# Kernel tuning notes

Measured on AMD Instinct MI355X. Metric: run time of the kernel, lower is better.

The kernel has to match this reference:

```python
import jax, jax.numpy as jnp
import numpy as np

B, Q, HIST, HID, NH, D, BS, NBLK, NUMB = 8, 512, 1536, 4096, 32, 128, 64, 32, 256


def _rope(x, pos):
    # GPT-NeoX-style rotary used by Falcon: rotate_half over full head_dim.
    Dh = x.shape[-1]
    inv = 1.0 / (10000.0 ** (jnp.arange(0, Dh, 2, dtype=jnp.float32) / Dh))  # [D/2]
    ang = pos.astype(jnp.float32)[:, None] * inv[None, :]                    # [T, D/2]
    cos = jnp.concatenate([jnp.cos(ang), jnp.cos(ang)], -1)[None, :, None, :]
    sin = jnp.concatenate([jnp.sin(ang), jnp.sin(ang)], -1)[None, :, None, :]
    half = Dh // 2
    rot = jnp.concatenate([-x[..., half:], x[..., :half]], -1)
    return x * cos + rot * sin


def setup_inputs() -> dict:
    key = jax.random.key(0)
    ks = jax.random.split(key, 6)
    hidden_states = jax.random.normal(ks[0], (1, B * Q, HID), jnp.float32) * 0.02
    qkv_weight = jax.random.normal(ks[1], ((NH + 2) * D, HID), jnp.float32) * 0.02
    dense_weight = jax.random.normal(ks[2], (HID, NH * D), jnp.float32) * 0.02
    past_key = jax.random.normal(ks[3], (NUMB, BS, 1, D), jnp.float32) * 0.02
    past_value = jax.random.normal(ks[4], (NUMB, BS, 1, D), jnp.float32) * 0.02
    q_start_loc = (jnp.arange(B) * Q).astype(jnp.int32)
    q_seq_length = jnp.full((B,), Q, jnp.int32)
    history_lengths = jnp.full((B,), HIST, jnp.int32)
    # each sequence owns NBLK distinct cache blocks (shuffled block table)
    block_offsets = jax.random.permutation(ks[5], NUMB).reshape(B, NBLK).astype(jnp.int32)
    position_ids_1d = (history_lengths[:, None] + jnp.arange(Q, dtype=jnp.int32)[None, :]).reshape(-1)
    return dict(hidden_states=hidden_states, qkv_weight=qkv_weight, dense_weight=dense_weight,
                past_key=past_key, past_value=past_value, q_start_loc=q_start_loc,
                q_seq_length=q_seq_length, history_lengths=history_lengths,
                block_offsets=block_offsets, position_ids_1d=position_ids_1d)


def reference(hidden_states, qkv_weight, dense_weight, past_key, past_value,
              q_start_loc, q_seq_length, history_lengths, block_offsets, position_ids_1d):
    T = hidden_states.shape[1]
    Bn = block_offsets.shape[0]
    Qn = T // Bn
    Dh = past_key.shape[-1]
    BSz = past_key.shape[1]
    # fused QKV projection
    fused = hidden_states @ qkv_weight.T                      # [1, T, (NH+2)*D]
    NHh = fused.shape[-1] // Dh - 2
    qkv = fused.reshape(1, T, NHh + 2, Dh)
    q = qkv[:, :, :NHh]                                       # [1, T, NH, D]
    k = qkv[:, :, NHh:NHh + 1]                                 # [1, T, 1, D]
    v = qkv[:, :, NHh + 1:]                                    # [1, T, 1, D]
    # inline rotary embedding on q, k
    q = _rope(q, position_ids_1d)
    k = _rope(k, position_ids_1d)
    # fill_kv_cache: scatter new K/V into paged cache via block table
    seq_id = jnp.repeat(jnp.arange(Bn), Qn)                   # [T]
    pos = position_ids_1d.astype(jnp.int32)                   # absolute kv position
    blk = block_offsets[seq_id, pos // BSz]                   # [T] physical block id
    off = pos % BSz
    past_key = past_key.at[blk, off].set(k.reshape(T, 1, Dh))
    past_value = past_value.at[blk, off].set(v.reshape(T, 1, Dh))
    # paged_attention_fwd: gather per-sequence K/V from paged cache
    KVc = block_offsets.shape[1] * BSz                        # kv capacity == kv_len here
    kseq = past_key[block_offsets].reshape(Bn, KVc, Dh)       # [B, KV, D] (1 kv head squeezed)
    vseq = past_value[block_offsets].reshape(Bn, KVc, Dh)
    qb = q.reshape(Bn, Qn, NHh, Dh)
    scale = 1.0 / jnp.sqrt(jnp.float32(Dh))
    scores = jnp.einsum('bqhd,bkd->bhqk', qb, kseq) * scale   # [B, H, Q, KV]
    qpos = history_lengths[:, None] + jnp.arange(Qn)[None, :] # [B, Q]
    mask = jnp.arange(KVc)[None, None, :] <= qpos[:, :, None] # causal + length mask
    scores = jnp.where(mask[:, None, :, :], scores, jnp.float32(-1e30))
    attn = jax.nn.softmax(scores, axis=-1)
    out = jnp.einsum('bhqk,bkd->bqhd', attn, vseq)            # [B, Q, H, D]
    out = out.reshape(1, T, NHh * Dh)
    return out @ dense_weight.T                                # [1, T, hidden]
```

## Files before the change

kernel.cpp:

```cpp
#include <hip/hip_runtime.h>

typedef __attribute__((ext_vector_type(8))) short bf16x8;
typedef __attribute__((ext_vector_type(4))) float f32x4;
typedef __attribute__((ext_vector_type(16))) float f32x16;
typedef __attribute__((ext_vector_type(2))) unsigned int u32x2;

constexpr int B_ = 8, Q_ = 512, HIST_ = 1536, HID_ = 4096, NH_ = 32, D_ = 128;
constexpr int BS_ = 64, NBLK_ = 32;
constexpr int T_ = B_ * Q_;
constexpr int QKVN = (NH_ + 2) * D_;
constexpr int KVC = NBLK_ * BS_;

__device__ __forceinline__ unsigned short f2bf(float f) {
  union { float f; unsigned u; } v; v.f = f;
  unsigned r = v.u + 0x7FFFu + ((v.u >> 16) & 1u);
  return (unsigned short)(r >> 16);
}
__device__ __forceinline__ float bf2f(unsigned short s) {
  union { unsigned u; float f; } v; v.u = ((unsigned)s) << 16;
  return v.f;
}
__device__ __forceinline__ int cvtpk_bf16(float lo, float hi) {
  int r;
  asm("v_cvt_pk_bf16_f32 %0, %1, %2" : "=v"(r) : "v"(lo), "v"(hi));
  return r;
}

__global__ void k_conv(const float* __restrict__ in, unsigned short* __restrict__ out, int n4) {
  int i = blockIdx.x * blockDim.x + threadIdx.x;
  int stride = gridDim.x * blockDim.x;
  for (; i < n4; i += stride) {
    float4 v = reinterpret_cast<const float4*>(in)[i];
    ushort4 o;
    o.x = f2bf(v.x); o.y = f2bf(v.y); o.z = f2bf(v.z); o.w = f2bf(v.w);
    reinterpret_cast<ushort4*>(out)[i] = o;
  }
}

__global__ __launch_bounds__(512, 2) void k_gemm256(const unsigned short* __restrict__ A,
                          const unsigned short* __restrict__ Bm,
                          float* __restrict__ Cf, unsigned short* __restrict__ Cb,
                          int MB, int K, int ldc) {
  extern __shared__ unsigned short smem[];
  unsigned short* sA = smem;
  unsigned short* sB = smem + 32768;
  const int tid = threadIdx.x, lane = tid & 63, w = tid >> 6;
  const int wr = w >> 2, wc = w & 3;
  const int lr = lane & 15, lk = lane >> 4;

  const int nwg = gridDim.x, orig = blockIdx.x;
  const int q8 = nwg >> 3, r8 = nwg & 7, xcd = orig & 7;
  const int wg = (xcd < r8 ? xcd * (q8 + 1) : r8 * (q8 + 1) + (xcd - r8) * q8) + (orig >> 3);
  const int m0 = (wg % MB) * 256;
  const int n0 = (wg / MB) * 256;
  const int NT = K >> 6;

  f32x4 acc[8][4];
#pragma unroll
  for (int mf = 0; mf < 8; ++mf)
#pragma unroll
    for (int nf = 0; nf < 4; ++nf) acc[mf][nf] = f32x4{0.f, 0.f, 0.f, 0.f};

  auto stage = [&](const unsigned short* __restrict__ Mat, int rbase, unsigned short* regionBase,
                   int ts, int half) {
    const int di = ts < NT ? ts : NT - 1;
    const size_t k0 = (size_t)di << 6;
    char* hb = (char*)(regionBase + (ts & 1) * 16384 + half * 8192);
#pragma unroll
    for (int c = 0; c < 2; ++c) {
      const int ob = c * 8192 + (w << 10) + (lane << 4);
      const int row = ob >> 7;
      const int sl = ((ob >> 4) & 7) ^ (row & 7);
      const unsigned short* src = Mat + (size_t)(rbase + half * 128 + row) * K + k0 + sl * 8;
      __builtin_amdgcn_global_load_lds((const __attribute__((address_space(1))) void*)src,
          (__attribute__((address_space(3))) void*)(hb + c * 8192 + (w << 10)), 16, 0, 0);
    }
  };

  stage(A, m0, sA, 0, 0); stage(A, m0, sA, 0, 1);
  stage(Bm, n0, sB, 0, 0); stage(Bm, n0, sB, 0, 1);
  stage(Bm, n0, sB, 1, 0); stage(Bm, n0, sB, 1, 1);
  asm volatile("s_waitcnt vmcnt(4)" ::: "memory");
  __builtin_amdgcn_s_barrier();

  for (int t = 0; t < NT; ++t) {
    const int cur = t & 1;
    unsigned short* a_t = sA + cur * 16384 + wr * 8192;
    unsigned short* b_t = sB + cur * 16384 + (wc >> 1) * 8192;
    bf16x8 bfr[4][2];
#pragma unroll
    for (int p = 0; p < 4; ++p) {
      bf16x8 af[2][2];
#pragma unroll
      for (int m = 0; m < 2; ++m)
#pragma unroll
        for (int kk = 0; kk < 2; ++kk) {
          const int r = p * 32 + m * 16 + lr;
          af[m][kk] = *reinterpret_cast<bf16x8*>(&a_t[r * 64 + ((((kk << 2) + lk) ^ (r & 7)) << 3)]);
        }
      if (p == 0) {
#pragma unroll
        for (int n = 0; n < 4; ++n)
#pragma unroll
          for (int kk = 0; kk < 2; ++kk) {
            const int rb = (wc & 1) * 64 + n * 16 + lr;
            bfr[n][kk] = *reinterpret_cast<bf16x8*>(&b_t[rb * 64 + ((((kk << 2) + lk) ^ (rb & 7)) << 3)]);
          }
      }
      if (p == 0) stage(A, m0, sA, t + 1, 0);
      if (p == 1) { stage(A, m0, sA, t + 1, 1); stage(Bm, n0, sB, t + 2, 0); }
      if (p == 2) stage(Bm, n0, sB, t + 2, 1);
      asm volatile("" ::: "memory");
      __builtin_amdgcn_s_barrier();
      asm volatile("s_waitcnt lgkmcnt(0)" ::: "memory");
      __builtin_amdgcn_sched_barrier(0);
      __builtin_amdgcn_s_setprio(1);
#pragma unroll
      for (int m = 0; m < 2; ++m)
#pragma unroll
        for (int n = 0; n < 4; ++n)
#pragma unroll
          for (int kk = 0; kk < 2; ++kk)
            acc[p * 2 + m][n] = __builtin_amdgcn_mfma_f32_16x16x32_bf16(af[m][kk], bfr[n][kk], acc[p * 2 + m][n], 0, 0, 0);
      __builtin_amdgcn_s_setprio(0);
      if (p == 3) asm volatile("s_waitcnt vmcnt(4)" ::: "memory");
      asm volatile("" ::: "memory");
      __builtin_amdgcn_s_barrier();
    }
  }
  asm volatile("s_waitcnt vmcnt(0)" ::: "memory");

#pragma unroll
  for (int mf = 0; mf < 8; ++mf)
#pragma unroll
    for (int nf = 0; nf < 4; ++nf)
#pragma unroll
      for (int j = 0; j < 4; ++j) {
        const int rr = m0 + wr * 128 + mf * 16 + lk * 4 + j;
        const int cc = n0 + wc * 64 + nf * 16 + lr;
        if (Cb) Cb[(size_t)rr * ldc + cc] = f2bf(acc[mf][nf][j]);
        else Cf[(size_t)rr * ldc + cc] = acc[mf][nf][j];
      }
}

__global__ void k_rope(const unsigned short* __restrict__ fused,
                       const int* __restrict__ pos_ids,
                       unsigned short* __restrict__ qb,
                       unsigned short* __restrict__ kseq,
                       unsigned short* __restrict__ vtg) {
  int t = blockIdx.x;
  int d = threadIdx.x;
  int b = t >> 9, q = t & 511;
  int pos = pos_ids[t];
  __shared__ float cs[64], sn[64];
  if (d < 64) {
    float inv = powf(10000.f, -(float)d * (1.f / 64.f));
    float ang = (float)pos * inv;
    cs[d] = cosf(ang);
    sn[d] = sinf(ang);
  }
  __syncthreads();
  const float scale = 0.1275174313836907f;
  float c = cs[d & 63], s = sn[d & 63];
  const unsigned short* row = fused + (size_t)t * QKVN;
#pragma unroll 4
  for (int h = 0; h < NH_; ++h) {
    float x = bf2f(row[h * D_ + d]);
    float xr = (d < 64) ? -bf2f(row[h * D_ + d + 64]) : bf2f(row[h * D_ + d - 64]);
    qb[(((size_t)(b * NH_ + h)) * Q_ + q) * D_ + d] = f2bf((x * c + xr * s) * scale);
  }
  {
    float x = bf2f(row[NH_ * D_ + d]);
    float xr = (d < 64) ? -bf2f(row[NH_ * D_ + d + 64]) : bf2f(row[NH_ * D_ + d - 64]);
    kseq[((size_t)b * KVC + pos) * D_ + d] = f2bf(x * c + xr * s);
  }
  vtg[((size_t)b * D_ + d) * KVC + pos] = row[(NH_ + 1) * D_ + d];
}

__global__ void k_gather(const float* __restrict__ pk, const float* __restrict__ pv,
                         const int* __restrict__ bo,
                         unsigned short* __restrict__ kseq, unsigned short* __restrict__ vtg) {
  __shared__ unsigned short vl[64 * 140];
  const int ptile = blockIdx.x;
  const int b = ptile / (HIST_ / 64);
  const int p0 = (ptile % (HIST_ / 64)) * 64;
  const int tid = threadIdx.x;
  const int blk = bo[b * NBLK_ + (p0 >> 6)];
#pragma unroll
  for (int c = 0; c < 8; ++c) {
    int u = c * 256 + tid;
    int p = u >> 5, d4 = u & 31;
    size_t src = ((size_t)blk * BS_ + p) * D_ + d4 * 4;
    float4 kv = *reinterpret_cast<const float4*>(pk + src);
    ushort4 ko;
    ko.x = f2bf(kv.x); ko.y = f2bf(kv.y); ko.z = f2bf(kv.z); ko.w = f2bf(kv.w);
    *reinterpret_cast<ushort4*>(kseq + ((size_t)b * KVC + p0 + p) * D_ + d4 * 4) = ko;
    float4 vv = *reinterpret_cast<const float4*>(pv + src);
    ushort4 vo;
    vo.x = f2bf(vv.x); vo.y = f2bf(vv.y); vo.z = f2bf(vv.z); vo.w = f2bf(vv.w);
    *reinterpret_cast<ushort4*>(&vl[p * 140 + d4 * 4]) = vo;
  }
  __syncthreads();
#pragma unroll
  for (int c = 0; c < 4; ++c) {
    int u = c * 256 + tid;
    int d = u >> 3, pg = u & 7;
    bf16x8 vv8;
#pragma unroll
    for (int i = 0; i < 8; ++i) vv8[i] = (short)vl[(pg * 8 + i) * 140 + d];
    *reinterpret_cast<bf16x8*>(vtg + ((size_t)b * D_ + d) * KVC + p0 + pg * 8) = vv8;
  }
}

__global__ __launch_bounds__(512, 2) void k_attn(const unsigned short* __restrict__ qb,
                       const unsigned short* __restrict__ kseq,
                       const unsigned short* __restrict__ vtg,
                       const int* __restrict__ histL,
                       unsigned short* __restrict__ outb) {
  __shared__ alignas(16) unsigned short kl[2][64 * 128];
  __shared__ alignas(16) unsigned short vt[2][128 * 64];
  const int qt = blockIdx.x, hp = blockIdx.y, b = blockIdx.z;
  const int tid = threadIdx.x, lane = tid & 63, w = tid >> 6;
  const int H = lane >> 5, q = lane & 31;
  const int h = hp * 8 + w;
  const int q0 = qt * 32;
  const int hist = histL[b];
  const unsigned short* kseq_b = kseq + (size_t)b * KVC * D_;
  const unsigned short* vtg_b  = vtg + (size_t)b * D_ * KVC;

  const unsigned short* qrow = qb + (((size_t)(b * NH_ + h)) * Q_ + q0 + q) * D_;
  bf16x8 aq[8];
#pragma unroll
  for (int ds = 0; ds < 8; ++ds)
    aq[ds] = *reinterpret_cast<const bf16x8*>(qrow + ds * 16 + H * 8);

  f32x16 o[4];
#pragma unroll
  for (int db = 0; db < 4; ++db)
#pragma unroll
    for (int r = 0; r < 16; ++r) o[db][r] = 0.f;
  float m = -1e30f, l = 0.f;

  const int ntiles = (hist + q0 + 32 + 63) >> 6;

  auto STAGE = [&](int bufi, int kv0) {
#pragma unroll
    for (int c = 0; c < 2; ++c) {
      int ob = c * 8192 + tid * 16;
      int row = ob >> 8;
      int sp = (ob >> 4) & 15;
      const unsigned short* src = kseq_b + (size_t)(kv0 + row) * D_ + (((sp ^ (row & 15)) << 3));
      __builtin_amdgcn_global_load_lds((const __attribute__((address_space(1))) void*)src,
          (__attribute__((address_space(3))) void*)(&kl[bufi][c * 4096 + w * 512]), 16, 0, 0);
    }
#pragma unroll
    for (int c = 0; c < 2; ++c) {
      int ob = c * 8192 + tid * 16;
      int row = ob >> 7;
      int sp = (ob >> 4) & 7;
      const unsigned short* src = vtg_b + (size_t)row * KVC + kv0 + (((sp ^ (row & 7)) << 3));
      __builtin_amdgcn_global_load_lds((const __attribute__((address_space(1))) void*)src,
          (__attribute__((address_space(3))) void*)(&vt[bufi][c * 4096 + w * 512]), 16, 0, 0);
    }
  };

  STAGE(0, 0);
  __syncthreads();

  for (int it = 0; it < ntiles; ++it) {
    const int cur = it & 1;
    if (it + 1 < ntiles) STAGE(cur ^ 1, (it + 1) * 64);
    const unsigned short* kb = kl[cur];
    const unsigned short* vb = vt[cur];

    f32x16 sa = f32x16{0.f,0.f,0.f,0.f,0.f,0.f,0.f,0.f,0.f,0.f,0.f,0.f,0.f,0.f,0.f,0.f};
    f32x16 sb = sa, sc = sa, sd = sa;
#pragma unroll
    for (int ds = 0; ds < 4; ++ds) {
      const int sl = ((2 * ds + H) ^ (q & 15)) << 3;
      bf16x8 k0 = *reinterpret_cast<const bf16x8*>(kb + q * 128 + sl);
      bf16x8 k1 = *reinterpret_cast<const bf16x8*>(kb + (32 + q) * 128 + sl);
      sa = __builtin_amdgcn_mfma_f32_32x32x16_bf16(k0, aq[ds], sa, 0, 0, 0);
      sc = __builtin_amdgcn_mfma_f32_32x32x16_bf16(k1, aq[ds], sc, 0, 0, 0);
    }
#pragma unroll
    for (int ds = 4; ds < 8; ++ds) {
      const int sl = ((2 * ds + H) ^ (q & 15)) << 3;
      bf16x8 k0 = *reinterpret_cast<const bf16x8*>(kb + q * 128 + sl);
      bf16x8 k1 = *reinterpret_cast<const bf16x8*>(kb + (32 + q) * 128 + sl);
      sb = __builtin_amdgcn_mfma_f32_32x32x16_bf16(k0, aq[ds], sb, 0, 0, 0);
      sd = __builtin_amdgcn_mfma_f32_32x32x16_bf16(k1, aq[ds], sd, 0, 0, 0);
    }
    f32x16 s0 = sa + sb;
    f32x16 s1 = sc + sd;

    if (it == ntiles - 1) {
      const int limit = hist + q0 + q - it * 64 - 4 * H;
#pragma unroll
      for (int r = 0; r < 16; ++r) {
        const int koff = (r & 3) + 8 * ((r >> 2) & 1) + 16 * (r >> 3);
        if (koff > limit) s0[r] = -1e30f;
        if (32 + koff > limit) s1[r] = -1e30f;
      }
    }

    float pmax = s0[0];
#pragma unroll
    for (int r = 1; r < 16; ++r) pmax = fmaxf(pmax, s0[r]);
#pragma unroll
    for (int r = 0; r < 16; ++r) pmax = fmaxf(pmax, s1[r]);
    pmax = fmaxf(pmax, __shfl_xor(pmax, 32));
    if (__any(pmax > m + 11.54f)) {
      float mn = fmaxf(m, pmax);
      float al = exp2f(m - mn);
      m = mn;
      l *= al;
#pragma unroll
      for (int db = 0; db < 4; ++db)
#pragma unroll
        for (int r = 0; r < 16; ++r) o[db][r] *= al;
    }
    float rs = 0.f;
#pragma unroll
    for (int r = 0; r < 16; ++r) { s0[r] = exp2f(s0[r] - m); rs += s0[r]; }
#pragma unroll
    for (int r = 0; r < 16; ++r) { s1[r] = exp2f(s1[r] - m); rs += s1[r]; }
    rs += __shfl_xor(rs, 32);
    l += rs;

#pragma unroll
    for (int s = 0; s < 4; ++s) {
      float p0, p1, p2, p3, p4, p5, p6, p7;
      if (s == 0)      { p0=s0[0];p1=s0[1];p2=s0[2];p3=s0[3];p4=s0[4];p5=s0[5];p6=s0[6];p7=s0[7]; }
      else if (s == 1) { p0=s0[8];p1=s0[9];p2=s0[10];p3=s0[11];p4=s0[12];p5=s0[13];p6=s0[14];p7=s0[15]; }
      else if (s == 2) { p0=s1[0];p1=s1[1];p2=s1[2];p3=s1[3];p4=s1[4];p5=s1[5];p6=s1[6];p7=s1[7]; }
      else             { p0=s1[8];p1=s1[9];p2=s1[10];p3=s1[11];p4=s1[12];p5=s1[13];p6=s1[14];p7=s1[15]; }
      int c01 = cvtpk_bf16(p0, p1);
      int c23 = cvtpk_bf16(p2, p3);
      int c45 = cvtpk_bf16(p4, p5);
      int c67 = cvtpk_bf16(p6, p7);
      u32x2 rA = __builtin_amdgcn_permlane32_swap(c01, c45, false, false);
      u32x2 rB = __builtin_amdgcn_permlane32_swap(c23, c67, false, false);
      union { unsigned wds[4]; bf16x8 v; } uu;
      uu.wds[0] = rA[0]; uu.wds[1] = rB[0]; uu.wds[2] = rA[1]; uu.wds[3] = rB[1];
#pragma unroll
      for (int db = 0; db < 4; ++db) {
        const int row = db * 32 + q;
        bf16x8 vf = *reinterpret_cast<const bf16x8*>(vb + row * 64 + ((((2 * s + H) ^ (row & 7))) << 3));
        o[db] = __builtin_amdgcn_mfma_f32_32x32x16_bf16(vf, uu.v, o[db], 0, 0, 0);
      }
    }
    __syncthreads();
  }

  const float il = 1.f / l;
  unsigned short* orow = outb + (size_t)(b * Q_ + q0 + q) * (NH_ * D_) + h * D_;
#pragma unroll
  for (int db = 0; db < 4; ++db)
#pragma unroll
    for (int rr = 0; rr < 4; ++rr) {
      ushort4 st;
      st.x = f2bf(o[db][rr * 4 + 0] * il);
      st.y = f2bf(o[db][rr * 4 + 1] * il);
      st.z = f2bf(o[db][rr * 4 + 2] * il);
      st.w = f2bf(o[db][rr * 4 + 3] * il);
      *reinterpret_cast<ushort4*>(orow + db * 32 + rr * 8 + 4 * H) = st;
    }
}

extern "C" void kernel_launch(void* const* d_in, const int* in_sizes, int n_in,
                              void* d_out, int out_size, void* d_ws, size_t ws_size,
                              hipStream_t stream) {
  const float* hidden = (const float*)d_in[0];
  const float* qkvw   = (const float*)d_in[1];
  const float* densew = (const float*)d_in[2];
  const float* pk     = (const float*)d_in[3];
  const float* pv     = (const float*)d_in[4];
  const int* histL    = (const int*)d_in[7];
  const int* bo       = (const int*)d_in[8];
  const int* posids   = (const int*)d_in[9];
  float* out = (float*)d_out;

  char* ws = (char*)d_ws;
  unsigned short* ws_hidden = (unsigned short*)(ws);
  unsigned short* ws_w      = (unsigned short*)(ws + 33554432);
  unsigned short* ws_fused  = (unsigned short*)(ws + 69206016);
  unsigned short* ws_q      = (unsigned short*)(ws + 104857600);
  unsigned short* ws_k      = (unsigned short*)(ws + 138412032);
  unsigned short* ws_vt     = (unsigned short*)(ws + 142606336);
  unsigned short* ws_attn   = ws_hidden;

  k_conv<<<2048, 256, 0, stream>>>(hidden, ws_hidden, T_ * HID_ / 4);
  k_conv<<<2048, 256, 0, stream>>>(qkvw, ws_w, QKVN * HID_ / 4);
  k_gemm256<<<dim3((T_ / 256) * (QKVN / 256)), 512, 131072, stream>>>(
      ws_hidden, ws_w, nullptr, ws_fused, T_ / 256, HID_, QKVN);
  k_rope<<<T_, 128, 0, stream>>>(ws_fused, posids, ws_q, ws_k, ws_vt);
  k_gather<<<B_ * (HIST_ / 64), 256, 0, stream>>>(pk, pv, bo, ws_k, ws_vt);
  dim3 ga(Q_ / 32, NH_ / 8, B_);
  k_attn<<<ga, 512, 0, stream>>>(ws_q, ws_k, ws_vt, histL, ws_attn);
  k_conv<<<2048, 256, 0, stream>>>(densew, ws_w, HID_ * HID_ / 4);
  k_gemm256<<<dim3((T_ / 256) * (HID_ / 256)), 512, 131072, stream>>>(
      ws_attn, ws_w, out, nullptr, T_ / 256, HID_, HID_);
}
```

Baseline: 580.7 us.

## Software-pipeline B fragment LDS loads across tiles with double-buffered registers

Unrolls the GEMM k-loop by two and keeps two register sets of B fragments. The B fragments for the next k-tile are read from LDS during the third and fourth MFMA phases of the current tile, so the B reads no longer sit on the critical path at the start of each tile. The schedule for issuing global-to-LDS stages and the vmcnt waits is rearranged to match. The cost is extra VGPR pressure under the 512-thread, 2-block launch bound, which could cause spills, and a more fragile ordering between the LDS double buffer and the global loads.

After: 565.6 us. 1.03x faster.

```diff
diff --git a/kernel.cpp b/kernel.cpp
--- a/kernel.cpp
+++ b/kernel.cpp
@@ -36,6 +36,76 @@
     reinterpret_cast<ushort4*>(out)[i] = o;
   }
 }
+
+#define LDA4(af, cur_, qq)                                                              \
+  {                                                                                     \
+    const unsigned short* a_t = sA + (cur_) * 16384;                                    \
+    const int r0 = wr * 128 + (qq) * 32 + lr;                                           \
+    const int r1 = r0 + 16;                                                             \
+    af[0][0] = *(const bf16x8*)&a_t[r0 * 64 + ((lk ^ (r0 & 7)) << 3)];                  \
+    af[0][1] = *(const bf16x8*)&a_t[r0 * 64 + (((4 + lk) ^ (r0 & 7)) << 3)];            \
+    af[1][0] = *(const bf16x8*)&a_t[r1 * 64 + ((lk ^ (r1 & 7)) << 3)];                  \
+    af[1][1] = *(const bf16x8*)&a_t[r1 * 64 + (((4 + lk) ^ (r1 & 7)) << 3)];            \
+  }
+
+#define LDB2(dst, cur_, nn)                                                             \
+  {                                                                                     \
+    const unsigned short* b_t = sB + (cur_) * 16384;                                    \
+    const int rb = wc * 64 + (nn) * 16 + lr;                                            \
+    dst[nn][0] = *(const bf16x8*)&b_t[rb * 64 + ((lk ^ (rb & 7)) << 3)];                \
+    dst[nn][1] = *(const bf16x8*)&b_t[rb * 64 + (((4 + lk) ^ (rb & 7)) << 3)];          \
+  }
+
+#define MFMA16(qq, af, Bf)                                                              \
+  __builtin_amdgcn_s_setprio(1);                                                        \
+  acc[(qq)*2+0][0] = __builtin_amdgcn_mfma_f32_16x16x32_bf16(af[0][0], Bf[0][0], acc[(qq)*2+0][0], 0, 0, 0); \
+  acc[(qq)*2+0][1] = __builtin_amdgcn_mfma_f32_16x16x32_bf16(af[0][0], Bf[1][0], acc[(qq)*2+0][1], 0, 0, 0); \
+  acc[(qq)*2+0][2] = __builtin_amdgcn_mfma_f32_16x16x32_bf16(af[0][0], Bf[2][0], acc[(qq)*2+0][2], 0, 0, 0); \
+  acc[(qq)*2+0][3] = __builtin_amdgcn_mfma_f32_16x16x32_bf16(af[0][0], Bf[3][0], acc[(qq)*2+0][3], 0, 0, 0); \
+  acc[(qq)*2+1][0] = __builtin_amdgcn_mfma_f32_16x16x32_bf16(af[1][0], Bf[0][0], acc[(qq)*2+1][0], 0, 0, 0); \
+  acc[(qq)*2+1][1] = __builtin_amdgcn_mfma_f32_16x16x32_bf16(af[1][0], Bf[1][0], acc[(qq)*2+1][1], 0, 0, 0); \
+  acc[(qq)*2+1][2] = __builtin_amdgcn_mfma_f32_16x16x32_bf16(af[1][0], Bf[2][0], acc[(qq)*2+1][2], 0, 0, 0); \
+  acc[(qq)*2+1][3] = __builtin_amdgcn_mfma_f32_16x16x32_bf16(af[1][0], Bf[3][0], acc[(qq)*2+1][3], 0, 0, 0); \
+  acc[(qq)*2+0][0] = __builtin_amdgcn_mfma_f32_16x16x32_bf16(af[0][1], Bf[0][1], acc[(qq)*2+0][0], 0, 0, 0); \
+  acc[(qq)*2+0][1] = __builtin_amdgcn_mfma_f32_16x16x32_bf16(af[0][1], Bf[1][1], acc[(qq)*2+0][1], 0, 0, 0); \
+  acc[(qq)*2+0][2] = __builtin_amdgcn_mfma_f32_16x16x32_bf16(af[0][1], Bf[2][1], acc[(qq)*2+0][2], 0, 0, 0); \
+  acc[(qq)*2+0][3] = __builtin_amdgcn_mfma_f32_16x16x32_bf16(af[0][1], Bf[3][1], acc[(qq)*2+0][3], 0, 0, 0); \
+  acc[(qq)*2+1][0] = __builtin_amdgcn_mfma_f32_16x16x32_bf16(af[1][1], Bf[0][1], acc[(qq)*2+1][0], 0, 0, 0); \
+  acc[(qq)*2+1][1] = __builtin_amdgcn_mfma_f32_16x16x32_bf16(af[1][1], Bf[1][1], acc[(qq)*2+1][1], 0, 0, 0); \
+  acc[(qq)*2+1][2] = __builtin_amdgcn_mfma_f32_16x16x32_bf16(af[1][1], Bf[2][1], acc[(qq)*2+1][2], 0, 0, 0); \
+  acc[(qq)*2+1][3] = __builtin_amdgcn_mfma_f32_16x16x32_bf16(af[1][1], Bf[3][1], acc[(qq)*2+1][3], 0, 0, 0); \
+  __builtin_amdgcn_s_setprio(0);
+
+#define SYNC_IN                                                                         \
+  asm volatile("" ::: "memory");                                                        \
+  __builtin_amdgcn_s_barrier();                                                         \
+  asm volatile("s_waitcnt lgkmcnt(0)" ::: "memory");                                    \
+  __builtin_amdgcn_sched_barrier(0);
+
+#define SYNC_OUT                                                                        \
+  asm volatile("" ::: "memory");                                                        \
+  __builtin_amdgcn_s_barrier();
+
+#define TILE(t_, cur_, BCUR, BNEXT)                                                     \
+  {                                                                                     \
+    bf16x8 af[2][2];                                                                    \
+    LDA4(af, cur_, 0);                                                                  \
+    stage(A, m0, sA, (t_) + 1, 0);                                                      \
+    SYNC_IN; MFMA16(0, af, BCUR); SYNC_OUT;                                             \
+    LDA4(af, cur_, 1);                                                                  \
+    stage(A, m0, sA, (t_) + 1, 1);                                                      \
+    asm volatile("s_waitcnt vmcnt(4)" ::: "memory");                                    \
+    SYNC_IN; MFMA16(1, af, BCUR); SYNC_OUT;                                             \
+    LDA4(af, cur_, 2);                                                                  \
+    LDB2(BNEXT, (cur_) ^ 1, 0); LDB2(BNEXT, (cur_) ^ 1, 1);                             \
+    stage(Bm, n0, sB, (t_) + 2, 0);                                                     \
+    SYNC_IN; MFMA16(2, af, BCUR); SYNC_OUT;                                             \
+    LDA4(af, cur_, 3);                                                                  \
+    LDB2(BNEXT, (cur_) ^ 1, 2); LDB2(BNEXT, (cur_) ^ 1, 3);                             \
+    stage(Bm, n0, sB, (t_) + 2, 1);                                                     \
+    asm volatile("s_waitcnt vmcnt(4)" ::: "memory");                                    \
+    SYNC_IN; MFMA16(3, af, BCUR); SYNC_OUT;                                             \
+  }
 
 __global__ __launch_bounds__(512, 2) void k_gemm256(const unsigned short* __restrict__ A,
                           const unsigned short* __restrict__ Bm,
@@ -82,51 +152,12 @@
   stage(Bm, n0, sB, 1, 0); stage(Bm, n0, sB, 1, 1);
   asm volatile("s_waitcnt vmcnt(4)" ::: "memory");
   __builtin_amdgcn_s_barrier();
-
-  for (int t = 0; t < NT; ++t) {
-    const int cur = t & 1;
-    unsigned short* a_t = sA + cur * 16384 + wr * 8192;
-    unsigned short* b_t = sB + cur * 16384 + (wc >> 1) * 8192;
-    bf16x8 bfr[4][2];
-#pragma unroll
-    for (int p = 0; p < 4; ++p) {
-      bf16x8 af[2][2];
-#pragma unroll
-      for (int m = 0; m < 2; ++m)
-#pragma unroll
-        for (int kk = 0; kk < 2; ++kk) {
-          const int r = p * 32 + m * 16 + lr;
-          af[m][kk] = *reinterpret_cast<bf16x8*>(&a_t[r * 64 + ((((kk << 2) + lk) ^ (r & 7)) << 3)]);
-        }
-      if (p == 0) {
-#pragma unroll
-        for (int n = 0; n < 4; ++n)
-#pragma unroll
-          for (int kk = 0; kk < 2; ++kk) {
-            const int rb = (wc & 1) * 64 + n * 16 + lr;
-            bfr[n][kk] = *reinterpret_cast<bf16x8*>(&b_t[rb * 64 + ((((kk << 2) + lk) ^ (rb & 7)) << 3)]);
-          }
-      }
-      if (p == 0) stage(A, m0, sA, t + 1, 0);
-      if (p == 1) { stage(A, m0, sA, t + 1, 1); stage(Bm, n0, sB, t + 2, 0); }
-      if (p == 2) stage(Bm, n0, sB, t + 2, 1);
-      asm volatile("" ::: "memory");
-      __builtin_amdgcn_s_barrier();
-      asm volatile("s_waitcnt lgkmcnt(0)" ::: "memory");
-      __builtin_amdgcn_sched_barrier(0);
-      __builtin_amdgcn_s_setprio(1);
-#pragma unroll
-      for (int m = 0; m < 2; ++m)
-#pragma unroll
-        for (int n = 0; n < 4; ++n)
-#pragma unroll
-          for (int kk = 0; kk < 2; ++kk)
-            acc[p * 2 + m][n] = __builtin_amdgcn_mfma_f32_16x16x32_bf16(af[m][kk], bfr[n][kk], acc[p * 2 + m][n], 0, 0, 0);
-      __builtin_amdgcn_s_setprio(0);
-      if (p == 3) asm volatile("s_waitcnt vmcnt(4)" ::: "memory");
-      asm volatile("" ::: "memory");
-      __builtin_amdgcn_s_barrier();
-    }
+  bf16x8 bX[4][2], bY[4][2];
+  LDB2(bX, 0, 0); LDB2(bX, 0, 1); LDB2(bX, 0, 2); LDB2(bX, 0, 3);
+
+  for (int t = 0; t < NT; t += 2) {
+    TILE(t, 0, bX, bY)
+    TILE(t + 1, 1, bY, bX)
   }
   asm volatile("s_waitcnt vmcnt(0)" ::: "memory");
 
```
